# Optimization experiments

Hardware: AMD Instinct MI355X
Metric: run time of the kernel (lower is better)

The kernel has to match this reference:

```python
import jax, jax.numpy as jnp
import numpy as np

N_NODES = 100000
N_EDGES = 1600000
D_FEAT = 64


def setup_inputs() -> dict:
    key = jax.random.key(0)
    k1, k2, k3 = jax.random.split(key, 3)
    h = jax.random.normal(k1, (N_NODES, D_FEAT), dtype=jnp.float32)
    src = jax.random.randint(k2, (N_EDGES,), 0, N_NODES, dtype=jnp.int32)
    dst = jax.random.randint(k3, (N_EDGES,), 0, N_NODES, dtype=jnp.int32)
    edge_index = jnp.stack([src, dst], axis=0)  # [2, E]
    return {"h": h, "edge_index": edge_index}


def reference(h, edge_index):
    # EdgePassing: message = src node features (gather along edges)
    # Max_aggregation: per-dst-node max over incoming messages (segment max)
    src, dst = edge_index[0], edge_index[1]
    msgs = h[src]  # [E, D] gathered mailbox, never densified per-node
    agg = jax.ops.segment_max(msgs, dst, num_segments=N_NODES)  # [N, D]
    # DGL leaves nodes with no incoming messages at zero; segment_max yields -inf
    return jnp.where(jnp.isneginf(agg), jnp.zeros_like(agg), agg)
```

## Files before the change

kernel.cpp:

```cpp
#include <hip/hip_runtime.h>

#define D_FEAT 64
#define NEG_INF_BITS 0xFF800000u
#define ENC_NEG_INF  0x007FFFFFu
#define NPB 128
#define BSHIFT 7
#define BM_BLOCK 512
#define MAXB 1024

__device__ __forceinline__ unsigned enc_f32(float v) {
    unsigned b = __float_as_uint(v);
    return ((int)b >= 0) ? (b ^ 0x80000000u) : ~b;
}
__device__ __forceinline__ float dec_f32(unsigned u) {
    return (u & 0x80000000u) ? __uint_as_float(u ^ 0x80000000u) : __uint_as_float(~u);
}

__global__ void count_kernel(const int* __restrict__ dst, int* __restrict__ counts,
                             int E, int Te, int B) {
    __shared__ int lh[MAXB];
    for (int i = threadIdx.x; i < B; i += blockDim.x) lh[i] = 0;
    __syncthreads();
    int t = blockIdx.x;
    int beg = t * Te;
    int end = min(E, beg + Te);
    int nE = (end > beg) ? (end - beg) : 0;
    int n4 = nE >> 2;
    const int4* d4 = (const int4*)(dst + beg);
    for (int k = threadIdx.x; k < n4; k += blockDim.x) {
        int4 d = d4[k];
        atomicAdd(&lh[d.x >> BSHIFT], 1);
        atomicAdd(&lh[d.y >> BSHIFT], 1);
        atomicAdd(&lh[d.z >> BSHIFT], 1);
        atomicAdd(&lh[d.w >> BSHIFT], 1);
    }
    for (int i = beg + (n4 << 2) + threadIdx.x; i < end; i += blockDim.x)
        atomicAdd(&lh[dst[i] >> BSHIFT], 1);
    __syncthreads();
    for (int i = threadIdx.x; i < B; i += blockDim.x) counts[t * B + i] = lh[i];
}

__global__ void colscan_kernel(int* __restrict__ counts, int* __restrict__ hist,
                               int T, int B) {
    int w = (blockIdx.x * blockDim.x + threadIdx.x) >> 6;
    int lane = threadIdx.x & 63;
    if (w >= B) return;
    int b = w;
    int R = T >> 6;
    int v[4], pre[4];
    int base_t = lane * R;
    for (int r = 0; r < R; ++r) v[r] = counts[(base_t + r) * B + b];
    int s = 0;
    for (int r = 0; r < R; ++r) { pre[r] = s; s += v[r]; }
    int incl = s;
    for (int off = 1; off < 64; off <<= 1) {
        int tup = __shfl_up(incl, off);
        if (lane >= off) incl += tup;
    }
    int excl = incl - s;
    for (int r = 0; r < R; ++r) counts[(base_t + r) * B + b] = excl + pre[r];
    int total = __shfl(incl, 63);
    if (lane == 0) hist[b] = total;
}

__global__ void scan_kernel(const int* __restrict__ hist, int* __restrict__ bucket_start,
                            int B) {
    __shared__ int lds[MAXB];
    int tid = threadIdx.x;
    int v = (tid < B) ? hist[tid] : 0;
    lds[tid] = v;
    __syncthreads();
    for (int off = 1; off < MAXB; off <<= 1) {
        int t = (tid >= off) ? lds[tid - off] : 0;
        __syncthreads();
        lds[tid] += t;
        __syncthreads();
    }
    if (tid < B) {
        bucket_start[tid] = lds[tid] - v;
        if (tid == B - 1) bucket_start[B] = lds[tid];
    }
}

__global__ void place_kernel(const int* __restrict__ src, const int* __restrict__ dst,
                             const int* __restrict__ counts, const int* __restrict__ bucket_start,
                             unsigned* __restrict__ packed, int E, int Te, int B) {
    __shared__ int lcur[MAXB];
    int t = blockIdx.x;
    for (int i = threadIdx.x; i < B; i += blockDim.x)
        lcur[i] = bucket_start[i] + counts[t * B + i];
    __syncthreads();
    int beg = t * Te;
    int end = min(E, beg + Te);
    for (int i = beg + threadIdx.x; i < end; i += blockDim.x) {
        int d = dst[i];
        int b = d >> BSHIFT;
        int pos = atomicAdd(&lcur[b], 1);
        packed[pos] = (unsigned)src[i] | ((unsigned)(d & (NPB - 1)) << 17);
    }
}

__global__ void __launch_bounds__(BM_BLOCK)
bucket_max_kernel(const float* __restrict__ h,
                  const int* __restrict__ bucket_start,
                  const unsigned* __restrict__ packed,
                  float* __restrict__ out, int N) {
    __shared__ unsigned buf[NPB * D_FEAT];
    int b = blockIdx.x;
    int tid = threadIdx.x;
    int node0 = b << BSHIFT;
    int nvals = (min(NPB, N - node0)) * D_FEAT;

    for (int i = tid; i < NPB * D_FEAT; i += BM_BLOCK) buf[i] = ENC_NEG_INF;
    __syncthreads();

    int beg = bucket_start[b];
    int end = bucket_start[b + 1];
    int wid = tid >> 6;
    int lane = tid & 63;

    for (int base = beg + (wid << 6); base < end; base += BM_BLOCK) {
        int nk = min(64, end - base);
        unsigned p = (lane < nk) ? packed[base + lane] : 0u;
        int j = 0;
        for (; j + 8 <= nk; j += 8) {
            unsigned q[8];
            float v[8];
            #pragma unroll
            for (int k = 0; k < 8; ++k) q[k] = (unsigned)__shfl((int)p, j + k);
            #pragma unroll
            for (int k = 0; k < 8; ++k) v[k] = h[(q[k] & 0x1FFFFu) * D_FEAT + lane];
            #pragma unroll
            for (int k = 0; k < 8; ++k)
                atomicMax(&buf[(q[k] >> 17) * D_FEAT + lane], enc_f32(v[k]));
        }
        for (; j < nk; ++j) {
            unsigned pj = (unsigned)__shfl((int)p, j);
            float v = h[(pj & 0x1FFFFu) * D_FEAT + lane];
            atomicMax(&buf[(pj >> 17) * D_FEAT + lane], enc_f32(v));
        }
    }
    __syncthreads();

    for (int i = tid; i < nvals; i += BM_BLOCK) {
        unsigned u = buf[i];
        out[node0 * D_FEAT + i] = (u == ENC_NEG_INF) ? 0.0f : dec_f32(u);
    }
}

__global__ void init_out_kernel(uint4* __restrict__ out, int n4) {
    int i = blockIdx.x * blockDim.x + threadIdx.x;
    if (i < n4) {
        uint4 v;
        v.x = NEG_INF_BITS; v.y = NEG_INF_BITS; v.z = NEG_INF_BITS; v.w = NEG_INF_BITS;
        out[i] = v;
    }
}
__global__ void scatter_max_kernel(const float* __restrict__ h, const int* __restrict__ src,
                                   const int* __restrict__ dst, float* __restrict__ out, int E) {
    int gid = blockIdx.x * blockDim.x + threadIdx.x;
    int e = gid >> 6;
    if (e >= E) return;
    int lane = gid & 63;
    float v = h[src[e] * D_FEAT + lane];
    int* addr = (int*)(out + dst[e] * D_FEAT + lane);
    if (v >= 0.0f) atomicMax(addr, __float_as_int(v));
    else           atomicMin((unsigned int*)addr, __float_as_uint(v));
}
__global__ void finalize_kernel(float* __restrict__ out, int n) {
    int i = blockIdx.x * blockDim.x + threadIdx.x;
    if (i < n && __float_as_uint(out[i]) == NEG_INF_BITS) out[i] = 0.0f;
}

extern "C" void kernel_launch(void* const* d_in, const int* in_sizes, int n_in,
                              void* d_out, int out_size, void* d_ws, size_t ws_size,
                              hipStream_t stream) {
    const float* h = (const float*)d_in[0];
    const int* edge_index = (const int*)d_in[1];
    int E = in_sizes[1] / 2;
    const int* src = edge_index;
    const int* dst = edge_index + E;
    float* out = (float*)d_out;
    int N = out_size / D_FEAT;

    int B = (N + NPB - 1) >> BSHIFT;

    int T = 0;
    for (int cand = 256; cand >= 64; cand >>= 1) {
        size_t need = ((size_t)cand * B + B + (B + 1) + (size_t)E) * sizeof(int);
        if (ws_size >= need) { T = cand; break; }
    }

    if (N <= (1 << 17) && B <= MAXB && T > 0) {
        int* counts       = (int*)d_ws;
        int* hist         = counts + (size_t)T * B;
        int* bucket_start = hist + B;
        unsigned* packed  = (unsigned*)(bucket_start + B + 1);

        int Te = ((E + T - 1) / T + 3) & ~3;

        count_kernel<<<T, 512, 0, stream>>>(dst, counts, E, Te, B);
        int cs_blocks = (B * 64 + 511) / 512;
        colscan_kernel<<<cs_blocks, 512, 0, stream>>>(counts, hist, T, B);
        scan_kernel<<<1, MAXB, 0, stream>>>(hist, bucket_start, B);
        place_kernel<<<T, 512, 0, stream>>>(src, dst, counts, bucket_start, packed, E, Te, B);
        bucket_max_kernel<<<B, BM_BLOCK, 0, stream>>>(h, bucket_start, packed, out, N);
    } else {
        int n4 = out_size / 4;
        init_out_kernel<<<(n4 + 255) / 256, 256, 0, stream>>>((uint4*)out, n4);
        long long total = (long long)E * 64;
        scatter_max_kernel<<<(int)((total + 255) / 256), 256, 0, stream>>>(h, src, dst, out, E);
        finalize_kernel<<<(out_size + 255) / 256, 256, 0, stream>>>(out, out_size);
    }
}
```

Before: 163.5 us.

## Fuse bucket-sort preprocessing into one cooperative kernel with grid syncs

Merges the count, column-scan, bucket scan and placement kernels into one cooperative kernel of 128 blocks of 1024 threads, separated by grid-wide syncs. Each block redoes the small bucket-start scan itself instead of waiting on a separate single-block launch, and placement reads src with int4 vector loads. The aim is to remove three kernel launch boundaries and their gaps. In exchange it relies on cooperative launch and grid.sync, which cost something on their own, and it reduces the number of threads in the count and place phases.

New measurement: 204.0 us. 24.7% more time.

```diff
diff --git a/kernel.cpp b/kernel.cpp
--- a/kernel.cpp
+++ b/kernel.cpp
@@ -1,4 +1,7 @@
 #include <hip/hip_runtime.h>
+#include <hip/hip_cooperative_groups.h>
+
+namespace cg = cooperative_groups;
 
 #define D_FEAT 64
 #define NEG_INF_BITS 0xFF800000u
@@ -7,6 +10,9 @@
 #define BSHIFT 7
 #define BM_BLOCK 512
 #define MAXB 1024
+#define PP_BLOCK 1024
+#define PP_WAVES (PP_BLOCK / 64)
+#define PP_T 128
 
 __device__ __forceinline__ unsigned enc_f32(float v) {
     unsigned b = __float_as_uint(v);
@@ -16,87 +22,125 @@
     return (u & 0x80000000u) ? __uint_as_float(u ^ 0x80000000u) : __uint_as_float(~u);
 }
 
-__global__ void count_kernel(const int* __restrict__ dst, int* __restrict__ counts,
-                             int E, int Te, int B) {
-    __shared__ int lh[MAXB];
-    for (int i = threadIdx.x; i < B; i += blockDim.x) lh[i] = 0;
-    __syncthreads();
+__global__ void __launch_bounds__(PP_BLOCK)
+preprocess_kernel(const int* __restrict__ src, const int* __restrict__ dst,
+                  int* __restrict__ counts, int* __restrict__ hist,
+                  int* __restrict__ bucket_start, unsigned* __restrict__ packed,
+                  int E, int Te, int T, int B) {
+    cg::grid_group grid = cg::this_grid();
+    __shared__ int sm[MAXB];
+    __shared__ int part[PP_WAVES][64];
+    __shared__ int sscan[PP_BLOCK];
+
     int t = blockIdx.x;
+    int tid = threadIdx.x;
     int beg = t * Te;
     int end = min(E, beg + Te);
-    int nE = (end > beg) ? (end - beg) : 0;
-    int n4 = nE >> 2;
-    const int4* d4 = (const int4*)(dst + beg);
-    for (int k = threadIdx.x; k < n4; k += blockDim.x) {
-        int4 d = d4[k];
-        atomicAdd(&lh[d.x >> BSHIFT], 1);
-        atomicAdd(&lh[d.y >> BSHIFT], 1);
-        atomicAdd(&lh[d.z >> BSHIFT], 1);
-        atomicAdd(&lh[d.w >> BSHIFT], 1);
-    }
-    for (int i = beg + (n4 << 2) + threadIdx.x; i < end; i += blockDim.x)
-        atomicAdd(&lh[dst[i] >> BSHIFT], 1);
-    __syncthreads();
-    for (int i = threadIdx.x; i < B; i += blockDim.x) counts[t * B + i] = lh[i];
-}
-
-__global__ void colscan_kernel(int* __restrict__ counts, int* __restrict__ hist,
-                               int T, int B) {
-    int w = (blockIdx.x * blockDim.x + threadIdx.x) >> 6;
-    int lane = threadIdx.x & 63;
-    if (w >= B) return;
-    int b = w;
-    int R = T >> 6;
-    int v[4], pre[4];
-    int base_t = lane * R;
-    for (int r = 0; r < R; ++r) v[r] = counts[(base_t + r) * B + b];
-    int s = 0;
-    for (int r = 0; r < R; ++r) { pre[r] = s; s += v[r]; }
-    int incl = s;
-    for (int off = 1; off < 64; off <<= 1) {
-        int tup = __shfl_up(incl, off);
-        if (lane >= off) incl += tup;
-    }
-    int excl = incl - s;
-    for (int r = 0; r < R; ++r) counts[(base_t + r) * B + b] = excl + pre[r];
-    int total = __shfl(incl, 63);
-    if (lane == 0) hist[b] = total;
-}
-
-__global__ void scan_kernel(const int* __restrict__ hist, int* __restrict__ bucket_start,
-                            int B) {
-    __shared__ int lds[MAXB];
-    int tid = threadIdx.x;
+
+    for (int i = tid; i < B; i += PP_BLOCK) sm[i] = 0;
+    __syncthreads();
+    if ((E & 3) == 0) {
+        int n4 = (end > beg) ? ((end - beg) >> 2) : 0;
+        const int4* d4 = (const int4*)(dst + beg);
+        for (int k = tid; k < n4; k += PP_BLOCK) {
+            int4 d = d4[k];
+            atomicAdd(&sm[d.x >> BSHIFT], 1);
+            atomicAdd(&sm[d.y >> BSHIFT], 1);
+            atomicAdd(&sm[d.z >> BSHIFT], 1);
+            atomicAdd(&sm[d.w >> BSHIFT], 1);
+        }
+        for (int i = beg + (n4 << 2) + tid; i < end; i += PP_BLOCK)
+            atomicAdd(&sm[dst[i] >> BSHIFT], 1);
+    } else {
+        for (int i = beg + tid; i < end; i += PP_BLOCK)
+            atomicAdd(&sm[dst[i] >> BSHIFT], 1);
+    }
+    __syncthreads();
+    for (int i = tid; i < B; i += PP_BLOCK) counts[t * B + i] = sm[i];
+
+    grid.sync();
+
+    int nbc = (B + 63) >> 6;
+    if (t < nbc) {
+        int lane = tid & 63;
+        int wid = tid >> 6;
+        int b = (t << 6) + lane;
+        bool ok = b < B;
+        int Tc = (T + PP_WAVES - 1) / PP_WAVES;
+        int t0 = wid * Tc;
+        int t1 = min(T, t0 + Tc);
+        int s = 0;
+        if (ok) {
+            for (int tt = t0; tt < t1; ++tt) s += counts[tt * B + b];
+        }
+        part[wid][lane] = s;
+        __syncthreads();
+        int base = 0, total = 0;
+        #pragma unroll
+        for (int w = 0; w < PP_WAVES; ++w) {
+            int pv = part[w][lane];
+            if (w < wid) base += pv;
+            total += pv;
+        }
+        if (ok) {
+            if (wid == 0) hist[b] = total;
+            int run = base;
+            for (int tt = t0; tt < t1; ++tt) {
+                int v = counts[tt * B + b];
+                counts[tt * B + b] = run;
+                run += v;
+            }
+        }
+    }
+
+    grid.sync();
+
     int v = (tid < B) ? hist[tid] : 0;
-    lds[tid] = v;
-    __syncthreads();
-    for (int off = 1; off < MAXB; off <<= 1) {
-        int t = (tid >= off) ? lds[tid - off] : 0;
+    sscan[tid] = v;
+    __syncthreads();
+    for (int off = 1; off < PP_BLOCK; off <<= 1) {
+        int a = (tid >= off) ? sscan[tid - off] : 0;
         __syncthreads();
-        lds[tid] += t;
+        sscan[tid] += a;
         __syncthreads();
     }
-    if (tid < B) {
-        bucket_start[tid] = lds[tid] - v;
-        if (tid == B - 1) bucket_start[B] = lds[tid];
-    }
-}
-
-__global__ void place_kernel(const int* __restrict__ src, const int* __restrict__ dst,
-                             const int* __restrict__ counts, const int* __restrict__ bucket_start,
-                             unsigned* __restrict__ packed, int E, int Te, int B) {
-    __shared__ int lcur[MAXB];
-    int t = blockIdx.x;
-    for (int i = threadIdx.x; i < B; i += blockDim.x)
-        lcur[i] = bucket_start[i] + counts[t * B + i];
-    __syncthreads();
-    int beg = t * Te;
-    int end = min(E, beg + Te);
-    for (int i = beg + threadIdx.x; i < end; i += blockDim.x) {
-        int d = dst[i];
-        int b = d >> BSHIFT;
-        int pos = atomicAdd(&lcur[b], 1);
-        packed[pos] = (unsigned)src[i] | ((unsigned)(d & (NPB - 1)) << 17);
+    int incl = sscan[tid];
+    int excl = incl - v;
+    if (t == 0) {
+        if (tid < B) bucket_start[tid] = excl;
+        if (tid == B - 1) bucket_start[B] = incl;
+    }
+    __syncthreads();
+    if (tid < B) sm[tid] = excl + counts[t * B + tid];
+    __syncthreads();
+
+    if ((E & 3) == 0) {
+        int n4 = (end > beg) ? ((end - beg) >> 2) : 0;
+        const int4* d4 = (const int4*)(dst + beg);
+        const int4* s4 = (const int4*)(src + beg);
+        for (int k = tid; k < n4; k += PP_BLOCK) {
+            int4 d = d4[k];
+            int4 s = s4[k];
+            int p0 = atomicAdd(&sm[d.x >> BSHIFT], 1);
+            packed[p0] = (unsigned)s.x | ((unsigned)(d.x & (NPB - 1)) << 17);
+            int p1 = atomicAdd(&sm[d.y >> BSHIFT], 1);
+            packed[p1] = (unsigned)s.y | ((unsigned)(d.y & (NPB - 1)) << 17);
+            int p2 = atomicAdd(&sm[d.z >> BSHIFT], 1);
+            packed[p2] = (unsigned)s.z | ((unsigned)(d.z & (NPB - 1)) << 17);
+            int p3 = atomicAdd(&sm[d.w >> BSHIFT], 1);
+            packed[p3] = (unsigned)s.w | ((unsigned)(d.w & (NPB - 1)) << 17);
+        }
+        for (int i = beg + (n4 << 2) + tid; i < end; i += PP_BLOCK) {
+            int d = dst[i];
+            int pos = atomicAdd(&sm[d >> BSHIFT], 1);
+            packed[pos] = (unsigned)src[i] | ((unsigned)(d & (NPB - 1)) << 17);
+        }
+    } else {
+        for (int i = beg + tid; i < end; i += PP_BLOCK) {
+            int d = dst[i];
+            int pos = atomicAdd(&sm[d >> BSHIFT], 1);
+            packed[pos] = (unsigned)src[i] | ((unsigned)(d & (NPB - 1)) << 17);
+        }
     }
 }
 
@@ -184,14 +228,10 @@
     int N = out_size / D_FEAT;
 
     int B = (N + NPB - 1) >> BSHIFT;
-
-    int T = 0;
-    for (int cand = 256; cand >= 64; cand >>= 1) {
-        size_t need = ((size_t)cand * B + B + (B + 1) + (size_t)E) * sizeof(int);
-        if (ws_size >= need) { T = cand; break; }
-    }
-
-    if (N <= (1 << 17) && B <= MAXB && T > 0) {
+    int T = PP_T;
+    size_t need = ((size_t)T * B + B + (B + 1) + (size_t)E) * sizeof(int);
+
+    if (N <= (1 << 17) && B <= MAXB && ws_size >= need) {
         int* counts       = (int*)d_ws;
         int* hist         = counts + (size_t)T * B;
         int* bucket_start = hist + B;
@@ -199,11 +239,14 @@
 
         int Te = ((E + T - 1) / T + 3) & ~3;
 
-        count_kernel<<<T, 512, 0, stream>>>(dst, counts, E, Te, B);
-        int cs_blocks = (B * 64 + 511) / 512;
-        colscan_kernel<<<cs_blocks, 512, 0, stream>>>(counts, hist, T, B);
-        scan_kernel<<<1, MAXB, 0, stream>>>(hist, bucket_start, B);
-        place_kernel<<<T, 512, 0, stream>>>(src, dst, counts, bucket_start, packed, E, Te, B);
+        const int* src_p = src;
+        const int* dst_p = dst;
+        void* kargs[] = { (void*)&src_p, (void*)&dst_p, (void*)&counts, (void*)&hist,
+                          (void*)&bucket_start, (void*)&packed,
+                          (void*)&E, (void*)&Te, (void*)&T, (void*)&B };
+        hipLaunchCooperativeKernel((const void*)preprocess_kernel, dim3(T), dim3(PP_BLOCK),
+                                   kargs, 0, stream);
+
         bucket_max_kernel<<<B, BM_BLOCK, 0, stream>>>(h, bucket_start, packed, out, N);
     } else {
         int n4 = out_size / 4;
```
